# Optimization experiments

Measured on AMD Instinct MI355X. Metric: run time of the kernel, lower is better.

The kernel has to match this reference:

```python
import jax, jax.numpy as jnp
import numpy as np

N, E = 100000, 600000
IN_DIM, HID, OUT_DIM = 128, 128, 1
BN_EPS = 1e-5
L2_EPS = 1e-12


def setup_inputs() -> dict:
    key = jax.random.key(0)
    ks = jax.random.split(key, 12)

    def xavier(k, shape):
        fan_in, fan_out = shape[0], shape[1]
        lim = float(np.sqrt(6.0 / (fan_in + fan_out)))
        return jax.random.uniform(k, shape, jnp.float32, -lim, lim)

    return {
        'x': jax.random.normal(ks[0], (N, IN_DIM), jnp.float32),
        'edge_index': jax.random.randint(ks[1], (2, E), 0, N, jnp.int32),
        # SAGEConv layer 1: lin_l (neighbor, with bias), lin_r (root, no bias)
        'W1_l': xavier(ks[2], (IN_DIM, HID)),
        'b1_l': jnp.zeros((HID,), jnp.float32),
        'W1_r': xavier(ks[3], (IN_DIM, HID)),
        # BatchNorm1d(hidden)
        'bn_gamma': jnp.ones((HID,), jnp.float32),
        'bn_beta': jnp.zeros((HID,), jnp.float32),
        # SAGEConv layer 2
        'W2_l': xavier(ks[4], (HID, HID)),
        'b2_l': jnp.zeros((HID,), jnp.float32),
        'W2_r': xavier(ks[5], (HID, HID)),
        # fc on causal half of embedding
        'fc_W': xavier(ks[6], (HID // 2, OUT_DIM)),
        'fc_b': jnp.zeros((OUT_DIM,), jnp.float32),
    }


def _sage_conv(x, src, dst, W_l, b_l, W_r, n_nodes):
    # mean-aggregate neighbor features: messages x[src] scattered to dst
    msg = x[src]  # [E, d] gather
    agg = jax.ops.segment_sum(msg, dst, num_segments=n_nodes)  # [N, d]
    cnt = jax.ops.segment_sum(jnp.ones((src.shape[0],), x.dtype), dst,
                              num_segments=n_nodes)  # [N]
    mean = agg / jnp.maximum(cnt, 1.0)[:, None]
    out = mean @ W_l + b_l + x @ W_r  # lin_l(agg) + lin_r(x)
    # normalize=True -> row-wise L2 normalize (F.normalize, eps=1e-12)
    nrm = jnp.linalg.norm(out, axis=-1, keepdims=True)
    return out / jnp.maximum(nrm, L2_EPS)


def reference(x, edge_index, W1_l, b1_l, W1_r, bn_gamma, bn_beta,
              W2_l, b2_l, W2_r, fc_W, fc_b):
    src, dst = edge_index[0], edge_index[1]
    n_nodes = x.shape[0]

    h = _sage_conv(x, src, dst, W1_l, b1_l, W1_r, n_nodes)

    # transition: ReLU -> BatchNorm1d (batch stats) -> Dropout (eval: identity)
    h = jax.nn.relu(h)
    mu = jnp.mean(h, axis=0)
    var = jnp.var(h, axis=0)
    h = (h - mu) * jax.lax.rsqrt(var + BN_EPS) * bn_gamma + bn_beta

    embed = _sage_conv(h, src, dst, W2_l, b2_l, W2_r, n_nodes)

    half = embed.shape[1] // 2
    preds = (embed[:, :half] @ fc_W + fc_b).squeeze()  # [N]
    return preds, embed
```

## Files before the change

### kernel.cpp

```cpp
#include <hip/hip_runtime.h>
#include <hip/hip_bf16.h>
#include <stdint.h>

typedef __attribute__((ext_vector_type(8))) __bf16 bf16x8;
typedef __attribute__((ext_vector_type(4))) float  f32x4;

__device__ __forceinline__ float bflo(uint32_t p){ return __uint_as_float(p << 16); }
__device__ __forceinline__ float bfhi(uint32_t p){ return __uint_as_float(p & 0xffff0000u); }
__device__ __forceinline__ uint16_t f2bf(float f){
    uint32_t u = __float_as_uint(f);
    uint32_t r = (u + 0x7fffu + ((u >> 16) & 1u)) >> 16;
    return (uint16_t)r;
}
__device__ __forceinline__ uint32_t packbf(float a, float b){
    return (uint32_t)f2bf(a) | ((uint32_t)f2bf(b) << 16);
}
__device__ __forceinline__ f32x4 MFMA(bf16x8 a, bf16x8 b, f32x4 c){
    return __builtin_amdgcn_mfma_f32_16x16x32_bf16(a, b, c, 0, 0, 0);
}

#define MB_IDX(row, lane) ((size_t)(row) * 128 + 64 + (lane))

__global__ void k_deg(const int* __restrict__ dst, int* __restrict__ counts, int E){
    int e = blockIdx.x * 256 + threadIdx.x;
    if (e < E) atomicAdd(&counts[dst[e]], 1);
}

__global__ void k_scan1(const int* __restrict__ counts, int* __restrict__ bsums, int N){
    __shared__ int lds[256];
    int t = threadIdx.x;
    int base = blockIdx.x * 2048 + t * 8;
    int s = 0;
    #pragma unroll
    for (int i = 0; i < 8; ++i){ int idx = base + i; s += (idx < N) ? counts[idx] : 0; }
    lds[t] = s; __syncthreads();
    for (int off = 128; off > 0; off >>= 1){
        if (t < off) lds[t] += lds[t + off];
        __syncthreads();
    }
    if (t == 0) bsums[blockIdx.x] = lds[0];
}

__global__ void k_scan2(int* bsums, int NB){
    int run = 0;
    for (int i = 0; i < NB; ++i){ int v = bsums[i]; bsums[i] = run; run += v; }
}

__global__ void k_scan3(const int* __restrict__ counts, const int* __restrict__ bsums,
                        int* __restrict__ offs, int N){
    __shared__ int lds[256];
    int t = threadIdx.x;
    int base = blockIdx.x * 2048 + t * 8;
    int local[8];
    int s = 0;
    #pragma unroll
    for (int i = 0; i < 8; ++i){
        int idx = base + i;
        int v = (idx < N) ? counts[idx] : 0;
        local[i] = v; s += v;
    }
    lds[t] = s; __syncthreads();
    for (int off = 1; off < 256; off <<= 1){
        int v = (t >= off) ? lds[t - off] : 0;
        __syncthreads();
        lds[t] += v;
        __syncthreads();
    }
    int run = bsums[blockIdx.x] + (lds[t] - s);
    #pragma unroll
    for (int i = 0; i < 8; ++i){
        int idx = base + i;
        if (idx < N){ offs[idx] = run; run += local[i]; }
    }
}

__global__ void k_fill(const int* __restrict__ src, const int* __restrict__ dst,
                       const int* __restrict__ offs, int* __restrict__ cursor,
                       int* __restrict__ ssrc, int E){
    int e = blockIdx.x * 256 + threadIdx.x;
    if (e < E){
        int d = dst[e];
        int p = atomicAdd(&cursor[d], 1);
        ssrc[offs[d] + p] = src[e];
    }
}

__global__ __launch_bounds__(256) void k_x2bf(const float* __restrict__ X,
        uint32_t* __restrict__ XbfE, uint32_t* __restrict__ Xlo, int N){
    int i = blockIdx.x * 256 + threadIdx.x;
    if (i >= N * 64) return;
    int row = i >> 6, lane = i & 63;
    float2 v = *(const float2*)(X + (size_t)i * 2);
    uint16_t h0 = f2bf(v.x), h1 = f2bf(v.y);
    float r0 = v.x - __uint_as_float((uint32_t)h0 << 16);
    float r1 = v.y - __uint_as_float((uint32_t)h1 << 16);
    XbfE[(size_t)row * 128 + lane] = (uint32_t)h0 | ((uint32_t)h1 << 16);
    Xlo[(size_t)i] = packbf(r0, r1);
}

__global__ void k_wprep(const float* __restrict__ Wl, const float* __restrict__ Wr,
                        const float* __restrict__ scale,
                        uint16_t* __restrict__ Wpk){
    int idx = blockIdx.x * 256 + threadIdx.x;
    int c = idx >> 8, k = idx & 255;
    float v;
    if (k < 128){
        v = Wl[k * 128 + c];
    } else {
        v = Wr[(k - 128) * 128 + c];
        if (scale) v *= scale[k - 128];
    }
    uint16_t h = f2bf(v);
    float r = v - __uint_as_float((uint32_t)h << 16);
    int kt = k >> 5, kk = k & 31;
    size_t base = (size_t)kt * 8192 + (size_t)c * 32 + kk;
    Wpk[base]        = h;
    Wpk[base + 4096] = f2bf(r);
}

template<int MODE>
__global__ __launch_bounds__(256) void k_agg(
        const uint32_t* __restrict__ Src, int sstr,
        const int* __restrict__ offs, const int* __restrict__ counts,
        const int* __restrict__ ssrc,
        const float* __restrict__ bnscale, const float* __restrict__ bnshift,
        uint32_t* __restrict__ MbBase, int N){
    int lane = threadIdx.x & 63;
    int node = blockIdx.x * 4 + (threadIdx.x >> 6);
    if (node >= N) return;
    int cnt = counts[node];
    if (cnt < 0) cnt = 0;
    int off = offs[node];
    float a0 = 0.f, a1 = 0.f;
    int j = 0;
    for (; j + 4 <= cnt; j += 4){
        int s0 = ssrc[off + j];
        int s1 = ssrc[off + j + 1];
        int s2 = ssrc[off + j + 2];
        int s3 = ssrc[off + j + 3];
        s0 = (s0 < 0) ? 0 : ((s0 >= N) ? (N - 1) : s0);
        s1 = (s1 < 0) ? 0 : ((s1 >= N) ? (N - 1) : s1);
        s2 = (s2 < 0) ? 0 : ((s2 >= N) ? (N - 1) : s2);
        s3 = (s3 < 0) ? 0 : ((s3 >= N) ? (N - 1) : s3);
        uint32_t p0 = Src[(size_t)s0 * sstr + lane];
        uint32_t p1 = Src[(size_t)s1 * sstr + lane];
        uint32_t p2 = Src[(size_t)s2 * sstr + lane];
        uint32_t p3 = Src[(size_t)s3 * sstr + lane];
        a0 += bflo(p0) + bflo(p1) + bflo(p2) + bflo(p3);
        a1 += bfhi(p0) + bfhi(p1) + bfhi(p2) + bfhi(p3);
    }
    for (; j < cnt; ++j){
        int s = ssrc[off + j];
        s = (s < 0) ? 0 : ((s >= N) ? (N - 1) : s);
        uint32_t p = Src[(size_t)s * sstr + lane];
        a0 += bflo(p); a1 += bfhi(p);
    }
    float inv = 1.0f / fmaxf((float)cnt, 1.0f);
    a0 *= inv; a1 *= inv;
    if (MODE == 1){
        int c0 = lane * 2;
        float sh0 = (cnt > 0) ? bnshift[c0]     : 0.f;
        float sh1 = (cnt > 0) ? bnshift[c0 + 1] : 0.f;
        a0 = a0 * bnscale[c0]     + sh0;
        a1 = a1 * bnscale[c0 + 1] + sh1;
    }
    MbBase[MB_IDX(node, lane)] = packbf(a0, a1);
}

template<int MODE>
__global__ __launch_bounds__(256) void k_gemm(
        const uint32_t* Own,
        const uint32_t* OwnLo,
        const uint32_t* Mb,
        const uint32_t* __restrict__ Wpk,
        const float* __restrict__ bias,
        uint32_t* HbfOut,
        float* Emb,
        float* __restrict__ bnsum, float* __restrict__ bnsumsq,
        const float* __restrict__ fcW, const float* __restrict__ fcb,
        float* __restrict__ preds, int N){
    __shared__ uint32_t __align__(16) sB[2][4096];
    __shared__ float lsum[128], lsq[128];
    const int lane = threadIdx.x & 63;
    const int wid  = threadIdx.x >> 6;
    const int l15  = lane & 15;
    const int g    = lane >> 4;
    const int ostr = (MODE == 0) ? 128 : 64;
    const int rowb = blockIdx.x * 128 + wid * 32;

#define STAGE_KT(ktv, bufv) do {                                              \
        const uint32_t* gs_ = Wpk + (size_t)(ktv) * 4096 + wid * 1024 + lane * 4; \
        uint32_t* ls_ = &sB[bufv][wid * 1024];                                \
        __builtin_amdgcn_global_load_lds(gs_,       ls_,       16, 0, 0);     \
        __builtin_amdgcn_global_load_lds(gs_ + 256, ls_ + 256, 16, 0, 0);     \
        __builtin_amdgcn_global_load_lds(gs_ + 512, ls_ + 512, 16, 0, 0);     \
        __builtin_amdgcn_global_load_lds(gs_ + 768, ls_ + 768, 16, 0, 0);     \
    } while (0)

    STAGE_KT(0, 0);
    if (MODE == 0){
        if (threadIdx.x < 128){ lsum[threadIdx.x] = 0.f; lsq[threadIdx.x] = 0.f; }
    }
    __syncthreads();

    int ar0 = rowb + l15;      if (ar0 >= N) ar0 = N - 1;
    int ar1 = rowb + 16 + l15; if (ar1 >= N) ar1 = N - 1;

    const uint32_t* mp0 = Mb  + (size_t)ar0 * 128 + 64 + g * 4;
    const uint32_t* mp1 = Mb  + (size_t)ar1 * 128 + 64 + g * 4;
    const uint32_t* op0 = Own + (size_t)ar0 * ostr + g * 4;
    const uint32_t* op1 = Own + (size_t)ar1 * ostr + g * 4;

    f32x4 acc0[8], acc1[8];
    const f32x4 zero = {0.f, 0.f, 0.f, 0.f};
    #pragma unroll
    for (int t = 0; t < 8; ++t){ acc0[t] = zero; acc1[t] = zero; }

    #pragma unroll
    for (int kt = 0; kt < 8; ++kt){
        const int cur = kt & 1;
        if (kt < 7) STAGE_KT(kt + 1, cur ^ 1);

        bf16x8 a0, a1, x0, x1;
        if (kt < 4){
            a0 = *(const bf16x8*)(mp0 + kt * 16);
            a1 = *(const bf16x8*)(mp1 + kt * 16);
        } else {
            a0 = *(const bf16x8*)(op0 + (kt - 4) * 16);
            a1 = *(const bf16x8*)(op1 + (kt - 4) * 16);
            if (MODE == 0){
                x0 = *(const bf16x8*)(OwnLo + (size_t)ar0 * 64 + g * 4 + (kt - 4) * 16);
                x1 = *(const bf16x8*)(OwnLo + (size_t)ar1 * 64 + g * 4 + (kt - 4) * 16);
            }
        }

        const uint32_t* sbase = &sB[cur][0];
        #pragma unroll
        for (int t = 0; t < 8; ++t){
            const uint32_t* bp = sbase + (t * 16 + l15) * 16 + g * 4;
            bf16x8 bh = *(const bf16x8*)bp;
            bf16x8 bl = *(const bf16x8*)(bp + 2048);
            acc0[t] = MFMA(a0, bh, acc0[t]);
            acc1[t] = MFMA(a1, bh, acc1[t]);
            if (MODE == 0 && kt >= 4){
                acc0[t] = MFMA(x0, bh, acc0[t]);
                acc1[t] = MFMA(x1, bh, acc1[t]);
            }
            acc0[t] = MFMA(a0, bl, acc0[t]);
            acc1[t] = MFMA(a1, bl, acc1[t]);
        }
        __syncthreads();
    }
#undef STAGE_KT

    float bv[8];
    #pragma unroll
    for (int t = 0; t < 8; ++t) bv[t] = bias[t * 16 + l15];

    float fw[4]; float fb = 0.f;
    if (MODE == 1){
        #pragma unroll
        for (int t = 0; t < 4; ++t) fw[t] = fcW[t * 16 + l15];
        fb = fcb[0];
    }

    float pbs[8], pbq[8];
    #pragma unroll
    for (int t = 0; t < 8; ++t){ pbs[t] = 0.f; pbq[t] = 0.f; }

    #pragma unroll
    for (int m = 0; m < 2; ++m){
        #pragma unroll
        for (int j = 0; j < 4; ++j){
            int orow = rowb + m * 16 + 4 * g + j;
            bool valid = orow < N;
            float o[8]; float ss = 0.f;
            #pragma unroll
            for (int t = 0; t < 8; ++t){
                o[t] = (m == 0 ? acc0[t][j] : acc1[t][j]) + bv[t];
                ss += o[t] * o[t];
            }
            ss += __shfl_xor(ss, 1, 64);
            ss += __shfl_xor(ss, 2, 64);
            ss += __shfl_xor(ss, 4, 64);
            ss += __shfl_xor(ss, 8, 64);
            float inv = 1.0f / fmaxf(sqrtf(ss), 1e-12f);
            if (MODE == 0){
                #pragma unroll
                for (int t = 0; t < 8; ++t){
                    float v = fmaxf(o[t] * inv, 0.f);
                    float pv = __shfl_xor(v, 1, 64);
                    if (valid){
                        pbs[t] += v; pbq[t] += v * v;
                        if (!(lane & 1))
                            HbfOut[(size_t)orow * 64 + t * 8 + (l15 >> 1)] = packbf(v, pv);
                    }
                }
            } else {
                float p = 0.f;
                #pragma unroll
                for (int t = 0; t < 8; ++t){
                    float v = o[t] * inv;
                    if (valid) Emb[(size_t)orow * 128 + t * 16 + l15] = v;
                    if (t < 4) p += v * fw[t];
                }
                p += __shfl_xor(p, 1, 64);
                p += __shfl_xor(p, 2, 64);
                p += __shfl_xor(p, 4, 64);
                p += __shfl_xor(p, 8, 64);
                if (valid && l15 == 0) preds[orow] = p + fb;
            }
        }
    }

    if (MODE == 0){
        #pragma unroll
        for (int t = 0; t < 8; ++t){
            pbs[t] += __shfl_xor(pbs[t], 16, 64);
            pbs[t] += __shfl_xor(pbs[t], 32, 64);
            pbq[t] += __shfl_xor(pbq[t], 16, 64);
            pbq[t] += __shfl_xor(pbq[t], 32, 64);
        }
        if (lane < 16){
            #pragma unroll
            for (int t = 0; t < 8; ++t){
                atomicAdd(&lsum[t * 16 + lane], pbs[t]);
                atomicAdd(&lsq [t * 16 + lane], pbq[t]);
            }
        }
        __syncthreads();
        if (threadIdx.x < 128){
            atomicAdd(&bnsum[threadIdx.x],   lsum[threadIdx.x]);
            atomicAdd(&bnsumsq[threadIdx.x], lsq[threadIdx.x]);
        }
    }
}

__global__ void k_bnfinal(const float* __restrict__ bnsum, const float* __restrict__ bnsumsq,
                          const float* __restrict__ gamma, const float* __restrict__ beta,
                          const float* __restrict__ W2r, const float* __restrict__ b2,
                          float* __restrict__ scale, float* __restrict__ shift,
                          float* __restrict__ bias2, int N){
    __shared__ float sh_l[128];
    int t = threadIdx.x;
    float invN = 1.0f / (float)N;
    float mu  = bnsum[t] * invN;
    float var = fmaxf(bnsumsq[t] * invN - mu * mu, 0.f);
    float istd = 1.0f / sqrtf(var + 1e-5f);
    float sc = gamma[t] * istd;
    float sf = beta[t] - mu * sc;
    scale[t] = sc; shift[t] = sf; sh_l[t] = sf;
    __syncthreads();
    float acc = b2[t];
    for (int k = 0; k < 128; ++k) acc += sh_l[k] * W2r[k * 128 + t];
    bias2[t] = acc;
}

__global__ void k_sent(float* __restrict__ preds, int N, float val){
    int i = blockIdx.x * 256 + threadIdx.x;
    if (i < N) preds[i] = val;
}

extern "C" void kernel_launch(void* const* d_in, const int* in_sizes, int n_in,
                              void* d_out, int out_size, void* d_ws, size_t ws_size,
                              hipStream_t stream){
    const int N = in_sizes[0] / 128;
    const int E = in_sizes[1] / 2;

    const float* x    = (const float*)d_in[0];
    const int*   ei   = (const int*)d_in[1];
    const int*   src  = ei;
    const int*   dst  = ei + E;
    const float* W1l  = (const float*)d_in[2];
    const float* b1   = (const float*)d_in[3];
    const float* W1r  = (const float*)d_in[4];
    const float* gam  = (const float*)d_in[5];
    const float* bet  = (const float*)d_in[6];
    const float* W2l  = (const float*)d_in[7];
    const float* b2   = (const float*)d_in[8];
    const float* W2r  = (const float*)d_in[9];
    const float* fcW  = (const float*)d_in[10];
    const float* fcb  = (const float*)d_in[11];

    float* preds = (float*)d_out;
    float* Emb   = preds + N;
    uint32_t* EmbU = (uint32_t*)Emb;

    char* w = (char*)d_ws;
    auto carve = [&](size_t bytes){ char* p = w; w += (bytes + 255) & ~(size_t)255; return p; };
    int*   counts  = (int*)  carve((size_t)N * 4);
    int*   offs    = (int*)  carve((size_t)N * 4);
    int*   cursor  = (int*)  carve((size_t)N * 4);
    int*   bsums   = (int*)  carve(256 * 4);
    float* bnsum   = (float*)carve(128 * 4);
    float* bnsumsq = (float*)carve(128 * 4);
    float* bnscale = (float*)carve(128 * 4);
    float* bnshift = (float*)carve(128 * 4);
    float* bias2   = (float*)carve(128 * 4);
    int*   ssrc    = (int*)  carve((size_t)E * 4);
    uint32_t* HbfXlo = (uint32_t*)carve((size_t)N * 256);
    uint16_t* Wpk1 = (uint16_t*)carve(131072);
    uint16_t* Wpk2 = (uint16_t*)carve(131072);
    size_t need = (size_t)(w - (char*)d_ws);
    if (ws_size < need){
        float val = 1024.f + 4.f * (float)((ws_size >> 20) > 255 ? 255 : (ws_size >> 20));
        k_sent<<<(N + 255) / 256, 256, 0, stream>>>(preds, N, val);
        return;
    }

    hipMemsetAsync(counts, 0, (size_t)N * 4, stream);
    hipMemsetAsync(cursor, 0, (size_t)N * 4, stream);
    hipMemsetAsync(bnsum,  0, 1024, stream);

    const int eb = (E + 255) / 256;
    const int NB = (N + 2047) / 2048;
    const int ab = (N + 3) / 4;
    const int gb = (N + 127) / 128;
    const int xb = (N * 64 + 255) / 256;

    k_deg  <<<eb, 256, 0, stream>>>(dst, counts, E);
    k_scan1<<<NB, 256, 0, stream>>>(counts, bsums, N);
    k_scan2<<<1,    1, 0, stream>>>(bsums, NB);
    k_scan3<<<NB, 256, 0, stream>>>(counts, bsums, offs, N);
    k_fill <<<eb, 256, 0, stream>>>(src, dst, offs, cursor, ssrc, E);

    k_x2bf <<<xb, 256, 0, stream>>>(x, EmbU, HbfXlo, N);
    k_wprep<<<128, 256, 0, stream>>>(W1l, W1r, nullptr, Wpk1);

    k_agg<0> <<<ab, 256, 0, stream>>>(EmbU, 128, offs, counts, ssrc,
                                      nullptr, nullptr, EmbU, N);
    k_gemm<0><<<gb, 256, 0, stream>>>(EmbU, HbfXlo, EmbU, (const uint32_t*)Wpk1, b1,
                                      HbfXlo, nullptr, bnsum, bnsumsq,
                                      nullptr, nullptr, nullptr, N);
    k_bnfinal<<<1, 128, 0, stream>>>(bnsum, bnsumsq, gam, bet, W2r, b2,
                                     bnscale, bnshift, bias2, N);
    k_wprep<<<128, 256, 0, stream>>>(W2l, W2r, bnscale, Wpk2);

    k_agg<1> <<<ab, 256, 0, stream>>>(HbfXlo, 64, offs, counts, ssrc,
                                      bnscale, bnshift, EmbU, N);
    k_gemm<1><<<gb, 256, 0, stream>>>(HbfXlo, nullptr, EmbU, (const uint32_t*)Wpk2, bias2,
                                      nullptr, Emb, nullptr, nullptr,
                                      fcW, fcb, preds, N);
}
```

Baseline: 380.8 us.

## Restage GEMM weights as swizzled hi/lo halves with A fragments preloaded

The weight packing now XOR-swizzles the 16-byte groups within each column to avoid LDS bank conflicts. The GEMM loads all 8 k-tiles of the high bf16 weight half into LDS at once, runs every high-half MFMA, then reloads the low half and runs those. This replaces per-k-tile double buffering. All A fragments are preloaded into registers up front, and launch bounds request 2 blocks per SM. The BN partial-sum scratch now reuses the weight LDS buffer. Together these cut per-k-tile barriers and bank conflicts, at the cost of more registers and a serialized second weight load.

```diff
diff --git a/kernel.cpp b/kernel.cpp
--- a/kernel.cpp
+++ b/kernel.cpp
@@ -113,7 +113,9 @@
     uint16_t h = f2bf(v);
     float r = v - __uint_as_float((uint32_t)h << 16);
     int kt = k >> 5, kk = k & 31;
-    size_t base = (size_t)kt * 8192 + (size_t)c * 32 + kk;
+    int g = kk >> 3, e = kk & 7;
+    int slot = (c << 2) | (g ^ ((c >> 1) & 3));
+    size_t base = (size_t)kt * 8192 + (size_t)slot * 8 + e;
     Wpk[base]        = h;
     Wpk[base + 4096] = f2bf(r);
 }
@@ -167,8 +169,20 @@
     MbBase[MB_IDX(node, lane)] = packbf(a0, a1);
 }
 
+__device__ __forceinline__ void stage_sel(const uint32_t* Wpk, uint32_t (*sB)[2048],
+                                          int wid, int lane, int sel){
+    #pragma unroll
+    for (int i = 0; i < 16; ++i){
+        int ch = wid * 16 + i;
+        int ktv = ch >> 3, part = ch & 7;
+        __builtin_amdgcn_global_load_lds(
+            Wpk + ktv * 4096 + sel * 2048 + part * 256 + lane * 4,
+            &sB[ktv][part * 256], 16, 0, 0);
+    }
+}
+
 template<int MODE>
-__global__ __launch_bounds__(256) void k_gemm(
+__global__ __launch_bounds__(256, 2) void k_gemm(
         const uint32_t* Own,
         const uint32_t* OwnLo,
         const uint32_t* Mb,
@@ -179,29 +193,16 @@
         float* __restrict__ bnsum, float* __restrict__ bnsumsq,
         const float* __restrict__ fcW, const float* __restrict__ fcb,
         float* __restrict__ preds, int N){
-    __shared__ uint32_t __align__(16) sB[2][4096];
-    __shared__ float lsum[128], lsq[128];
+    __shared__ uint32_t __align__(16) sB[8][2048];
     const int lane = threadIdx.x & 63;
     const int wid  = threadIdx.x >> 6;
     const int l15  = lane & 15;
     const int g    = lane >> 4;
+    const int gx4  = (g ^ ((l15 >> 1) & 3)) * 4;
     const int ostr = (MODE == 0) ? 128 : 64;
     const int rowb = blockIdx.x * 128 + wid * 32;
 
-#define STAGE_KT(ktv, bufv) do {                                              \
-        const uint32_t* gs_ = Wpk + (size_t)(ktv) * 4096 + wid * 1024 + lane * 4; \
-        uint32_t* ls_ = &sB[bufv][wid * 1024];                                \
-        __builtin_amdgcn_global_load_lds(gs_,       ls_,       16, 0, 0);     \
-        __builtin_amdgcn_global_load_lds(gs_ + 256, ls_ + 256, 16, 0, 0);     \
-        __builtin_amdgcn_global_load_lds(gs_ + 512, ls_ + 512, 16, 0, 0);     \
-        __builtin_amdgcn_global_load_lds(gs_ + 768, ls_ + 768, 16, 0, 0);     \
-    } while (0)
-
-    STAGE_KT(0, 0);
-    if (MODE == 0){
-        if (threadIdx.x < 128){ lsum[threadIdx.x] = 0.f; lsq[threadIdx.x] = 0.f; }
-    }
-    __syncthreads();
+    stage_sel(Wpk, sB, wid, lane, 0);
 
     int ar0 = rowb + l15;      if (ar0 >= N) ar0 = N - 1;
     int ar1 = rowb + 16 + l15; if (ar1 >= N) ar1 = N - 1;
@@ -211,47 +212,61 @@
     const uint32_t* op0 = Own + (size_t)ar0 * ostr + g * 4;
     const uint32_t* op1 = Own + (size_t)ar1 * ostr + g * 4;
 
+    bf16x8 am0[4], am1[4], ao0[4], ao1[4];
+    #pragma unroll
+    for (int q = 0; q < 4; ++q){
+        am0[q] = *(const bf16x8*)(mp0 + q * 16);
+        am1[q] = *(const bf16x8*)(mp1 + q * 16);
+        ao0[q] = *(const bf16x8*)(op0 + q * 16);
+        ao1[q] = *(const bf16x8*)(op1 + q * 16);
+    }
+    bf16x8 xl0[4], xl1[4];
+    if (MODE == 0){
+        #pragma unroll
+        for (int q = 0; q < 4; ++q){
+            xl0[q] = *(const bf16x8*)(OwnLo + (size_t)ar0 * 64 + g * 4 + q * 16);
+            xl1[q] = *(const bf16x8*)(OwnLo + (size_t)ar1 * 64 + g * 4 + q * 16);
+        }
+    }
+
     f32x4 acc0[8], acc1[8];
     const f32x4 zero = {0.f, 0.f, 0.f, 0.f};
     #pragma unroll
     for (int t = 0; t < 8; ++t){ acc0[t] = zero; acc1[t] = zero; }
 
+    __syncthreads();
+
     #pragma unroll
     for (int kt = 0; kt < 8; ++kt){
-        const int cur = kt & 1;
-        if (kt < 7) STAGE_KT(kt + 1, cur ^ 1);
-
-        bf16x8 a0, a1, x0, x1;
-        if (kt < 4){
-            a0 = *(const bf16x8*)(mp0 + kt * 16);
-            a1 = *(const bf16x8*)(mp1 + kt * 16);
-        } else {
-            a0 = *(const bf16x8*)(op0 + (kt - 4) * 16);
-            a1 = *(const bf16x8*)(op1 + (kt - 4) * 16);
-            if (MODE == 0){
-                x0 = *(const bf16x8*)(OwnLo + (size_t)ar0 * 64 + g * 4 + (kt - 4) * 16);
-                x1 = *(const bf16x8*)(OwnLo + (size_t)ar1 * 64 + g * 4 + (kt - 4) * 16);
-            }
-        }
-
-        const uint32_t* sbase = &sB[cur][0];
+        bf16x8 a0 = (kt < 4) ? am0[kt] : ao0[kt - 4];
+        bf16x8 a1 = (kt < 4) ? am1[kt] : ao1[kt - 4];
         #pragma unroll
         for (int t = 0; t < 8; ++t){
-            const uint32_t* bp = sbase + (t * 16 + l15) * 16 + g * 4;
-            bf16x8 bh = *(const bf16x8*)bp;
-            bf16x8 bl = *(const bf16x8*)(bp + 2048);
+            bf16x8 bh = *(const bf16x8*)(&sB[kt][(t * 16 + l15) * 16 + gx4]);
             acc0[t] = MFMA(a0, bh, acc0[t]);
             acc1[t] = MFMA(a1, bh, acc1[t]);
             if (MODE == 0 && kt >= 4){
-                acc0[t] = MFMA(x0, bh, acc0[t]);
-                acc1[t] = MFMA(x1, bh, acc1[t]);
+                acc0[t] = MFMA(xl0[kt - 4], bh, acc0[t]);
+                acc1[t] = MFMA(xl1[kt - 4], bh, acc1[t]);
             }
+        }
+    }
+
+    __syncthreads();
+    stage_sel(Wpk, sB, wid, lane, 1);
+    __syncthreads();
+
+    #pragma unroll
+    for (int kt = 0; kt < 8; ++kt){
+        bf16x8 a0 = (kt < 4) ? am0[kt] : ao0[kt - 4];
+        bf16x8 a1 = (kt < 4) ? am1[kt] : ao1[kt - 4];
+        #pragma unroll
+        for (int t = 0; t < 8; ++t){
+            bf16x8 bl = *(const bf16x8*)(&sB[kt][(t * 16 + l15) * 16 + gx4]);
             acc0[t] = MFMA(a0, bl, acc0[t]);
             acc1[t] = MFMA(a1, bl, acc1[t]);
         }
-        __syncthreads();
-    }
-#undef STAGE_KT
+    }
 
     float bv[8];
     #pragma unroll
@@ -314,6 +329,8 @@
     }
 
     if (MODE == 0){
+        float* lsum = (float*)&sB[0][0];
+        float* lsq  = lsum + 128;
         #pragma unroll
         for (int t = 0; t < 8; ++t){
             pbs[t] += __shfl_xor(pbs[t], 16, 64);
@@ -321,6 +338,9 @@
             pbq[t] += __shfl_xor(pbq[t], 16, 64);
             pbq[t] += __shfl_xor(pbq[t], 32, 64);
         }
+        __syncthreads();
+        if (threadIdx.x < 128){ lsum[threadIdx.x] = 0.f; lsq[threadIdx.x] = 0.f; }
+        __syncthreads();
         if (lane < 16){
             #pragma unroll
             for (int t = 0; t < 8; ++t){
```

After: 376.5 us. Within noise of the previous version (-1.1%).
